# Kernel tuning notes

Measured on AMD Instinct MI355X. Metric: run time of the kernel, lower is better.

## Reference

```python
import jax, jax.numpy as jnp
import numpy as np

N = 100000   # nodes
E = 6400000  # edges (avg degree 64)
F = 512      # num_features
C = 16       # num_classes

def _glorot(key, shape):
    fan_in, fan_out = shape
    lim = (6.0 / (fan_in + fan_out)) ** 0.5
    return jax.random.uniform(key, shape, jnp.float32, -lim, lim)

def setup_inputs() -> dict:
    key = jax.random.key(0)
    ks = jax.random.split(key, 8)
    x = jax.random.normal(ks[0], (N, F), jnp.float32)
    edge_index = jax.random.randint(ks[1], (2, E), 0, N, dtype=jnp.int64)
    return {
        "x": x,
        "edge_index": edge_index,
        "W1": _glorot(ks[2], (F, 16)), "b1": jnp.zeros((16,), jnp.float32),
        "W2": _glorot(ks[3], (16, 32)), "b2": jnp.zeros((32,), jnp.float32),
        "W3": _glorot(ks[4], (32, C)),  "b3": jnp.zeros((C,), jnp.float32),
        "Wc": _glorot(ks[5], (C, C)),   "bc": jnp.zeros((C,), jnp.float32),
    }

def _gcn_conv(x, row, col, norm, W, b):
    # PyG GCNConv: transform, then normalized sum-aggregation, then bias
    h = x @ W                                   # [N, out]
    msg = h[row] * norm[:, None]                # gather + scale, [E+N, out]
    agg = jax.ops.segment_sum(msg, col, num_segments=N)
    return agg + b

def reference(x, edge_index, W1, b1, W2, b2, W3, b3, Wc, bc):
    n = x.shape[0]
    loops = jnp.arange(n, dtype=edge_index.dtype)
    row = jnp.concatenate([edge_index[0], loops])  # source
    col = jnp.concatenate([edge_index[1], loops])  # target
    # symmetric normalization D^{-1/2} A_hat D^{-1/2}
    deg = jax.ops.segment_sum(jnp.ones_like(col, dtype=x.dtype), col, num_segments=n)
    dis = jnp.where(deg > 0, jax.lax.rsqrt(deg), 0.0)
    norm = dis[row] * dis[col]                     # [E+N]
    h = jax.nn.relu(_gcn_conv(x, row, col, norm, W1, b1))
    h = jax.nn.relu(_gcn_conv(h, row, col, norm, W2, b2))
    h = jax.nn.relu(_gcn_conv(h, row, col, norm, W3, b3))
    out = h @ Wc + bc
    return (out, h)
```

## Files before the change

### kernel.cpp

```cpp
#include <hip/hip_runtime.h>
#include <hip/hip_bf16.h>
#include <hip/hip_fp16.h>
#include <stdint.h>


#define MS_CHUNK 15360

__device__ __forceinline__ int blockScanExclusive256(int v, int* wsum) {
  int lane = threadIdx.x & 63;
  int wid  = threadIdx.x >> 6;
  int inc = v;
#pragma unroll
  for (int d = 1; d < 64; d <<= 1) {
    int y = __shfl_up(inc, d, 64);
    if (lane >= d) inc += y;
  }
  if (lane == 63) wsum[wid] = inc;
  __syncthreads();
  if (threadIdx.x == 0) {
    int s = 0;
#pragma unroll
    for (int w = 0; w < 4; ++w) { int t = wsum[w]; wsum[w] = s; s += t; }
  }
  __syncthreads();
  return inc - v + wsum[wid];
}

__device__ __forceinline__ int blockScanExclusive512(int v, int* wsum) {
  int lane = threadIdx.x & 63;
  int wid  = threadIdx.x >> 6;
  int inc = v;
#pragma unroll
  for (int d = 1; d < 64; d <<= 1) {
    int y = __shfl_up(inc, d, 64);
    if (lane >= d) inc += y;
  }
  if (lane == 63) wsum[wid] = inc;
  __syncthreads();
  if (threadIdx.x == 0) {
    int s = 0;
#pragma unroll
    for (int w = 0; w < 8; ++w) { int t = wsum[w]; wsum[w] = s; s += t; }
  }
  __syncthreads();
  return inc - v + wsum[wid];
}

__global__ __launch_bounds__(256) void k_bscan(const int* __restrict__ counts,
                                               int* __restrict__ bbase,
                                               int nb, int etot) {
  __shared__ int wsum[4];
  __shared__ int carry_s;
  if (threadIdx.x == 0) carry_s = 0;
  __syncthreads();
  for (int base = 0; base < nb; base += 256) {
    int i = base + threadIdx.x;
    int v = (i < nb) ? counts[i] : 0;
    int ex = blockScanExclusive256(v, wsum);
    int c = carry_s;
    __syncthreads();
    if (i < nb) bbase[i] = ex + c;
    if (threadIdx.x == 255) carry_s = c + ex + v;
    __syncthreads();
  }
  if (threadIdx.x == 0) bbase[nb] = etot;
}

__global__ __launch_bounds__(256) void k_scatter1(
    const int* __restrict__ erow, const int* __restrict__ ecol,
    int* __restrict__ cursor, unsigned* __restrict__ sorted,
    int e, int chunk, int nb, int cap) {
  __shared__ unsigned staging[MS_CHUNK];
  __shared__ int lstart[256];
  __shared__ int lfill[256];
  __shared__ int gbase[256];
  __shared__ int wsum[4];
  int g = blockIdx.x;
  int s0 = g * chunk;
  int s1 = min(e, s0 + chunk);
  lfill[threadIdx.x] = 0;
  __syncthreads();
  {
    int i = s0 + threadIdx.x;
    for (; i + 768 < s1; i += 1024) {
      int c0 = ecol[i], c1 = ecol[i + 256], c2 = ecol[i + 512], c3 = ecol[i + 768];
      atomicAdd(&lfill[c0 >> 9], 1);
      atomicAdd(&lfill[c1 >> 9], 1);
      atomicAdd(&lfill[c2 >> 9], 1);
      atomicAdd(&lfill[c3 >> 9], 1);
    }
    for (; i < s1; i += 256) atomicAdd(&lfill[ecol[i] >> 9], 1);
  }
  __syncthreads();
  int cnt = lfill[threadIdx.x];
  int ex = blockScanExclusive256(cnt, wsum);
  lstart[threadIdx.x] = ex;
  int gb = 0;
  if (threadIdx.x < nb && cnt > 0) gb = atomicAdd(&cursor[threadIdx.x], cnt);
  gbase[threadIdx.x] = gb;
  __syncthreads();
  lfill[threadIdx.x] = 0;
  __syncthreads();
  {
    int i = s0 + threadIdx.x;
    for (; i + 768 < s1; i += 1024) {
      int c0 = ecol[i],       c1 = ecol[i + 256], c2 = ecol[i + 512], c3 = ecol[i + 768];
      int r0 = erow[i],       r1 = erow[i + 256], r2 = erow[i + 512], r3 = erow[i + 768];
      int b0 = c0 >> 9, b1 = c1 >> 9, b2 = c2 >> 9, b3 = c3 >> 9;
      int p0 = atomicAdd(&lfill[b0], 1);
      int p1 = atomicAdd(&lfill[b1], 1);
      int p2 = atomicAdd(&lfill[b2], 1);
      int p3 = atomicAdd(&lfill[b3], 1);
      staging[lstart[b0] + p0] = ((unsigned)r0 << 9) | (unsigned)(c0 & 511);
      staging[lstart[b1] + p1] = ((unsigned)r1 << 9) | (unsigned)(c1 & 511);
      staging[lstart[b2] + p2] = ((unsigned)r2 << 9) | (unsigned)(c2 & 511);
      staging[lstart[b3] + p3] = ((unsigned)r3 << 9) | (unsigned)(c3 & 511);
    }
    for (; i < s1; i += 256) {
      int c = ecol[i];
      int b = c >> 9;
      int p = atomicAdd(&lfill[b], 1);
      staging[lstart[b] + p] = ((unsigned)erow[i] << 9) | (unsigned)(c & 511);
    }
  }
  __syncthreads();
  int wid = threadIdx.x >> 6, L = threadIdx.x & 63;
  for (int b = wid; b < nb; b += 4) {
    int len = lfill[b];
    int ls = lstart[b];
    int gdst = b * cap + gbase[b];
    for (int j = L; j < len; j += 64)
      sorted[gdst + j] = staging[ls + j];
  }
}

__global__ __launch_bounds__(256) void k_transform1(
    const float* __restrict__ x, const float* __restrict__ W,
    __half* __restrict__ t1raw, int* __restrict__ cursor, int n) {
  if (blockIdx.x == 0) cursor[threadIdx.x] = 0;

  int L = threadIdx.x & 63;
  int wid = blockIdx.x * 4 + (threadIdx.x >> 6);
  int nw = gridDim.x * 4;

  float w[8][16];
  const float4* W4 = reinterpret_cast<const float4*>(W);
#pragma unroll
  for (int i = 0; i < 4; ++i) {
#pragma unroll
    for (int c4 = 0; c4 < 4; ++c4) {
      float4 va = W4[(4 * L + i) * 4 + c4];
      w[i][c4 * 4 + 0] = va.x; w[i][c4 * 4 + 1] = va.y;
      w[i][c4 * 4 + 2] = va.z; w[i][c4 * 4 + 3] = va.w;
      float4 vb = W4[(256 + 4 * L + i) * 4 + c4];
      w[4 + i][c4 * 4 + 0] = vb.x; w[4 + i][c4 * 4 + 1] = vb.y;
      w[4 + i][c4 * 4 + 2] = vb.z; w[4 + i][c4 * 4 + 3] = vb.w;
    }
  }
  int col = ((L & 1) << 3) | ((L & 2) << 1) | ((L & 4) >> 1) | ((L & 8) >> 3);

  for (int r = wid; r < n; r += nw) {
    const float4* xr = reinterpret_cast<const float4*>(x + (size_t)r * 512);
    float4 v0 = xr[L];
    float4 v1 = xr[64 + L];
    float acc[16];
#pragma unroll
    for (int c = 0; c < 16; ++c) {
      float a = v0.x * w[0][c];
      a = fmaf(v0.y, w[1][c], a);
      a = fmaf(v0.z, w[2][c], a);
      a = fmaf(v0.w, w[3][c], a);
      a = fmaf(v1.x, w[4][c], a);
      a = fmaf(v1.y, w[5][c], a);
      a = fmaf(v1.z, w[6][c], a);
      a = fmaf(v1.w, w[7][c], a);
      acc[c] = a;
    }
#pragma unroll
    for (int j = 0; j < 8; ++j) {
      float send = (L & 1) ? acc[j] : acc[j + 8];
      float recv = __shfl_xor(send, 1, 64);
      acc[j] = ((L & 1) ? acc[j + 8] : acc[j]) + recv;
    }
#pragma unroll
    for (int j = 0; j < 4; ++j) {
      float send = (L & 2) ? acc[j] : acc[j + 4];
      float recv = __shfl_xor(send, 2, 64);
      acc[j] = ((L & 2) ? acc[j + 4] : acc[j]) + recv;
    }
#pragma unroll
    for (int j = 0; j < 2; ++j) {
      float send = (L & 4) ? acc[j] : acc[j + 2];
      float recv = __shfl_xor(send, 4, 64);
      acc[j] = ((L & 4) ? acc[j + 2] : acc[j]) + recv;
    }
    {
      float send = (L & 8) ? acc[0] : acc[1];
      float recv = __shfl_xor(send, 8, 64);
      acc[0] = ((L & 8) ? acc[1] : acc[0]) + recv;
    }
    float s = acc[0];
    s += __shfl_xor(s, 16, 64);
    s += __shfl_xor(s, 32, 64);
    if (L < 16) t1raw[r * 16 + col] = __float2half(s);
  }
}

__global__ __launch_bounds__(512) void k_pass2(const unsigned* __restrict__ sorted,
                                               const int* __restrict__ counts,
                                               const int* __restrict__ bbase,
                                               float* __restrict__ dis,
                                               int* __restrict__ rowptr,
                                               __half* __restrict__ t1,
                                               int* __restrict__ csr,
                                               int n, int etot, int cap) {
  __shared__ int hist[512];
  __shared__ int cur[512];
  __shared__ int wsum[8];
  int b = blockIdx.x;
  hist[threadIdx.x] = 0;
  __syncthreads();
  int s0 = b * cap;
  int s1 = s0 + counts[b];
  for (int i = s0 + threadIdx.x; i < s1; i += 512)
    atomicAdd(&hist[sorted[i] & 511], 1);
  __syncthreads();
  int j = threadIdx.x;
  int node = (b << 9) + j;
  int deg = hist[j];
  int ex = blockScanExclusive512(deg, wsum);
  float dv = rsqrtf((float)(deg + 1));
  int gpos = bbase[b] + ex;
  cur[j] = gpos;
  if (node < n) {
    dis[node] = dv;
    rowptr[node] = gpos;
    __half2* t2 = reinterpret_cast<__half2*>(t1 + ((size_t)node << 4));
#pragma unroll
    for (int q = 0; q < 8; ++q) {
      float2 fv = __half22float2(t2[q]);
      fv.x *= dv; fv.y *= dv;
      t2[q] = __float22half2_rn(fv);
    }
  }
  if (b == 0 && threadIdx.x == 0) rowptr[n] = etot;
  __syncthreads();
  for (int i = s0 + threadIdx.x; i < s1; i += 512) {
    unsigned v = sorted[i];
    int pos = atomicAdd(&cur[v & 511], 1);
    csr[pos] = (int)(v >> 9);
  }
}

__device__ __forceinline__ float gather16(const __half* __restrict__ hs,
                                          const int* __restrict__ rowptr,
                                          const int* __restrict__ csr,
                                          int node, int f) {
  int base = (int)(threadIdx.x & 48);
  float acc0 = __half2float(hs[(node << 4) + f]);
  int e0 = rowptr[node], e1 = rowptr[node + 1];
  int e = e0;
  float acc1 = 0.f, acc2 = 0.f, acc3 = 0.f;
  for (; e + 16 <= e1; e += 16) {
    int rr = csr[e + f];
    int r0  = __shfl(rr, base + 0, 64),  r1  = __shfl(rr, base + 1, 64);
    int r2  = __shfl(rr, base + 2, 64),  r3  = __shfl(rr, base + 3, 64);
    int r4  = __shfl(rr, base + 4, 64),  r5  = __shfl(rr, base + 5, 64);
    int r6  = __shfl(rr, base + 6, 64),  r7  = __shfl(rr, base + 7, 64);
    int r8  = __shfl(rr, base + 8, 64),  r9  = __shfl(rr, base + 9, 64);
    int r10 = __shfl(rr, base + 10, 64), r11 = __shfl(rr, base + 11, 64);
    int r12 = __shfl(rr, base + 12, 64), r13 = __shfl(rr, base + 13, 64);
    int r14 = __shfl(rr, base + 14, 64), r15 = __shfl(rr, base + 15, 64);
    __half v0  = hs[(r0  << 4) + f], v1  = hs[(r1  << 4) + f];
    __half v2  = hs[(r2  << 4) + f], v3  = hs[(r3  << 4) + f];
    __half v4  = hs[(r4  << 4) + f], v5  = hs[(r5  << 4) + f];
    __half v6  = hs[(r6  << 4) + f], v7  = hs[(r7  << 4) + f];
    __half v8  = hs[(r8  << 4) + f], v9  = hs[(r9  << 4) + f];
    __half v10 = hs[(r10 << 4) + f], v11 = hs[(r11 << 4) + f];
    __half v12 = hs[(r12 << 4) + f], v13 = hs[(r13 << 4) + f];
    __half v14 = hs[(r14 << 4) + f], v15 = hs[(r15 << 4) + f];
    acc0 += (__half2float(v0)  + __half2float(v1))  + (__half2float(v2)  + __half2float(v3));
    acc1 += (__half2float(v4)  + __half2float(v5))  + (__half2float(v6)  + __half2float(v7));
    acc2 += (__half2float(v8)  + __half2float(v9))  + (__half2float(v10) + __half2float(v11));
    acc3 += (__half2float(v12) + __half2float(v13)) + (__half2float(v14) + __half2float(v15));
  }
  for (; e + 4 <= e1; e += 4) {
    int r0 = csr[e + 0], r1 = csr[e + 1], r2 = csr[e + 2], r3 = csr[e + 3];
    float v0 = __half2float(hs[(r0 << 4) + f]), v1 = __half2float(hs[(r1 << 4) + f]);
    float v2 = __half2float(hs[(r2 << 4) + f]), v3 = __half2float(hs[(r3 << 4) + f]);
    acc0 += (v0 + v1) + (v2 + v3);
  }
  for (; e < e1; ++e) acc0 += __half2float(hs[(csr[e] << 4) + f]);
  return (acc0 + acc1) + (acc2 + acc3);
}

__global__ __launch_bounds__(256) void k_agg_rb(
    const __half* __restrict__ hs, const int* __restrict__ rowptr,
    const int* __restrict__ csr, const float* __restrict__ dis,
    const float* __restrict__ b, __half* __restrict__ out, int n) {
  int node = blockIdx.x * 16 + threadIdx.x / 16;
  int f = threadIdx.x % 16;
  if (node >= n) return;
  float acc = gather16(hs, rowptr, csr, node, f);
  float d = dis[node];
  float t = fmaxf(fmaf(d, acc, b[f]), 0.f);
  out[(node << 4) + f] = __float2half(t * d);
}

__global__ __launch_bounds__(256) void k_agg_mid(
    const __half* __restrict__ hs, const int* __restrict__ rowptr,
    const int* __restrict__ csr, const float* __restrict__ dis,
    const float* __restrict__ W2, const float* __restrict__ b2,
    const float* __restrict__ W3, __half* __restrict__ out, int n) {
  __shared__ float w2s[512];
  __shared__ float w3s[512];
  __shared__ float b2s[32];
  for (int i = threadIdx.x; i < 512; i += 256) { w2s[i] = W2[i]; w3s[i] = W3[i]; }
  if (threadIdx.x < 32) b2s[threadIdx.x] = b2[threadIdx.x];
  __syncthreads();
  int node = blockIdx.x * 16 + threadIdx.x / 16;
  int f = threadIdx.x % 16;
  if (node >= n) return;
  float acc = gather16(hs, rowptr, csr, node, f);
  float d = dis[node];
  float v = d * acc;
  int base = threadIdx.x & 48;
  float a0 = b2s[f], a1 = b2s[f + 16];
#pragma unroll
  for (int k = 0; k < 16; ++k) {
    float vk = __shfl(v, base + k, 64);
    a0 = fmaf(vk, w2s[k * 32 + f], a0);
    a1 = fmaf(vk, w2s[k * 32 + 16 + f], a1);
  }
  a0 = fmaxf(a0, 0.f);
  a1 = fmaxf(a1, 0.f);
  float t = 0.f;
#pragma unroll
  for (int c = 0; c < 16; ++c) {
    float h0 = __shfl(a0, base + c, 64);
    float h1 = __shfl(a1, base + c, 64);
    t = fmaf(h0, w3s[c * 16 + f], t);
    t = fmaf(h1, w3s[(c + 16) * 16 + f], t);
  }
  out[(node << 4) + f] = __float2half(t * d);
}

__global__ __launch_bounds__(256) void k_agg_out(
    const __half* __restrict__ hs, const int* __restrict__ rowptr,
    const int* __restrict__ csr, const float* __restrict__ dis,
    const float* __restrict__ b3, const float* __restrict__ Wc,
    const float* __restrict__ bc, float* __restrict__ outh,
    float* __restrict__ outc, int n) {
  __shared__ float wcs[256];
  __shared__ float b3s[16];
  __shared__ float bcs[16];
  if (threadIdx.x < 256) wcs[threadIdx.x] = Wc[threadIdx.x];
  if (threadIdx.x < 16) { b3s[threadIdx.x] = b3[threadIdx.x]; bcs[threadIdx.x] = bc[threadIdx.x]; }
  __syncthreads();
  int node = blockIdx.x * 16 + threadIdx.x / 16;
  int f = threadIdx.x % 16;
  if (node >= n) return;
  float acc = gather16(hs, rowptr, csr, node, f);
  float d = dis[node];
  float h = fmaxf(fmaf(d, acc, b3s[f]), 0.f);
  outh[(node << 4) + f] = h;
  int base = threadIdx.x & 48;
  float o = bcs[f];
#pragma unroll
  for (int k = 0; k < 16; ++k) {
    float hk = __shfl(h, base + k, 64);
    o = fmaf(hk, wcs[k * 16 + f], o);
  }
  outc[(node << 4) + f] = o;
}

extern "C" void kernel_launch(void* const* d_in, const int* in_sizes, int n_in,
                              void* d_out, int out_size, void* d_ws, size_t ws_size,
                              hipStream_t stream) {
  (void)n_in; (void)out_size;
  const float* x  = (const float*)d_in[0];
  const int*   ei = (const int*)d_in[1];
  const float* W1 = (const float*)d_in[2];
  const float* b1 = (const float*)d_in[3];
  const float* W2 = (const float*)d_in[4];
  const float* b2 = (const float*)d_in[5];
  const float* W3 = (const float*)d_in[6];
  const float* b3 = (const float*)d_in[7];
  const float* Wc = (const float*)d_in[8];
  const float* bc = (const float*)d_in[9];

  const int F = 512;
  int N = in_sizes[0] / F;
  int E = in_sizes[1] / 2;
  const int* erow = ei;
  const int* ecol = ei + E;
  int NB = (N + 511) >> 9;
  const int chunk = MS_CHUNK;
  int GS = (E + chunk - 1) / chunk;
  int CAP = ((E / NB) + 2048 + 511) & ~511;

  auto align = [](size_t v) { return (v + 255) & ~(size_t)255; };
  char* p = (char*)d_ws;
  int*   cursor = (int*)p;   p += align(256 * 4);
  int*   bbase  = (int*)p;   p += align(257 * 4);
  float* dis    = (float*)p; p += align((size_t)N * 4);
  int*   rowptr = (int*)p;   p += align(((size_t)N + 1) * 4);
  int*   csr    = (int*)p;   p += align((size_t)E * 4);
  unsigned* sorted = (unsigned*)p; p += align((size_t)NB * CAP * 4);
  __half* bufA = (__half*)p; p += align((size_t)N * 16 * 2);
  __half* bufB = (__half*)p; p += align((size_t)N * 16 * 2);
  if ((size_t)(p - (char*)d_ws) > ws_size) return;

  float* outc = (float*)d_out;
  float* outh = (float*)d_out + (size_t)N * 16;

  k_transform1<<<2048, 256, 0, stream>>>(x, W1, bufA, cursor, N);
  k_scatter1<<<GS, 256, 0, stream>>>(erow, ecol, cursor, sorted, E, chunk, NB, CAP);
  k_bscan<<<1, 256, 0, stream>>>(cursor, bbase, NB, E);
  k_pass2<<<NB, 512, 0, stream>>>(sorted, cursor, bbase, dis, rowptr, bufA, csr, N, E, CAP);

  k_agg_rb<<<(N + 15) / 16, 256, 0, stream>>>(bufA, rowptr, csr, dis, b1, bufB, N);
  k_agg_mid<<<(N + 15) / 16, 256, 0, stream>>>(bufB, rowptr, csr, dis, W2, b2, W3, bufA, N);
  k_agg_out<<<(N + 15) / 16, 256, 0, stream>>>(bufA, rowptr, csr, dis, b3, Wc, bc, outh, outc, N);
}
```

Before: 317.7 us.

## Assign one wavefront per node in aggregation kernels instead of 16 lanes

The three aggregation kernels now map a full 64-lane wavefront to each destination node, with four edge slots of 16 features processed per step, and combine the partial sums with xor shuffles. The old scheme gave each node 16 lanes and a serial loop over neighbours. The change aims to raise the number of gathers in flight per node and reduce the serial loop length for degree-64 nodes. In exchange, each block covers 4× fewer nodes, there are extra reduction shuffles, and only 16 of 64 lanes write results.

```diff
diff --git a/kernel.cpp b/kernel.cpp
--- a/kernel.cpp
+++ b/kernel.cpp
@@ -252,59 +252,45 @@
   }
 }
 
-__device__ __forceinline__ float gather16(const __half* __restrict__ hs,
-                                          const int* __restrict__ rowptr,
-                                          const int* __restrict__ csr,
-                                          int node, int f) {
-  int base = (int)(threadIdx.x & 48);
-  float acc0 = __half2float(hs[(node << 4) + f]);
+__device__ __forceinline__ float gather_wave(const __half* __restrict__ hs,
+                                             const int* __restrict__ rowptr,
+                                             const int* __restrict__ csr,
+                                             int node, int L) {
+  int f = L & 15;
+  int es = L >> 4;
   int e0 = rowptr[node], e1 = rowptr[node + 1];
-  int e = e0;
-  float acc1 = 0.f, acc2 = 0.f, acc3 = 0.f;
-  for (; e + 16 <= e1; e += 16) {
-    int rr = csr[e + f];
-    int r0  = __shfl(rr, base + 0, 64),  r1  = __shfl(rr, base + 1, 64);
-    int r2  = __shfl(rr, base + 2, 64),  r3  = __shfl(rr, base + 3, 64);
-    int r4  = __shfl(rr, base + 4, 64),  r5  = __shfl(rr, base + 5, 64);
-    int r6  = __shfl(rr, base + 6, 64),  r7  = __shfl(rr, base + 7, 64);
-    int r8  = __shfl(rr, base + 8, 64),  r9  = __shfl(rr, base + 9, 64);
-    int r10 = __shfl(rr, base + 10, 64), r11 = __shfl(rr, base + 11, 64);
-    int r12 = __shfl(rr, base + 12, 64), r13 = __shfl(rr, base + 13, 64);
-    int r14 = __shfl(rr, base + 14, 64), r15 = __shfl(rr, base + 15, 64);
-    __half v0  = hs[(r0  << 4) + f], v1  = hs[(r1  << 4) + f];
-    __half v2  = hs[(r2  << 4) + f], v3  = hs[(r3  << 4) + f];
-    __half v4  = hs[(r4  << 4) + f], v5  = hs[(r5  << 4) + f];
-    __half v6  = hs[(r6  << 4) + f], v7  = hs[(r7  << 4) + f];
-    __half v8  = hs[(r8  << 4) + f], v9  = hs[(r9  << 4) + f];
-    __half v10 = hs[(r10 << 4) + f], v11 = hs[(r11 << 4) + f];
-    __half v12 = hs[(r12 << 4) + f], v13 = hs[(r13 << 4) + f];
-    __half v14 = hs[(r14 << 4) + f], v15 = hs[(r15 << 4) + f];
-    acc0 += (__half2float(v0)  + __half2float(v1))  + (__half2float(v2)  + __half2float(v3));
-    acc1 += (__half2float(v4)  + __half2float(v5))  + (__half2float(v6)  + __half2float(v7));
-    acc2 += (__half2float(v8)  + __half2float(v9))  + (__half2float(v10) + __half2float(v11));
-    acc3 += (__half2float(v12) + __half2float(v13)) + (__half2float(v14) + __half2float(v15));
-  }
-  for (; e + 4 <= e1; e += 4) {
-    int r0 = csr[e + 0], r1 = csr[e + 1], r2 = csr[e + 2], r3 = csr[e + 3];
-    float v0 = __half2float(hs[(r0 << 4) + f]), v1 = __half2float(hs[(r1 << 4) + f]);
-    float v2 = __half2float(hs[(r2 << 4) + f]), v3 = __half2float(hs[(r3 << 4) + f]);
-    acc0 += (v0 + v1) + (v2 + v3);
-  }
-  for (; e < e1; ++e) acc0 += __half2float(hs[(csr[e] << 4) + f]);
-  return (acc0 + acc1) + (acc2 + acc3);
+  float a0 = 0.f, a1 = 0.f, a2 = 0.f, a3 = 0.f;
+  for (int e = e0; e < e1; e += 16) {
+    int m = e + f;
+    int rr = (m < e1) ? csr[m] : 0;
+    int s0i = __shfl(rr, es, 64);
+    int s1i = __shfl(rr, 4 + es, 64);
+    int s2i = __shfl(rr, 8 + es, 64);
+    int s3i = __shfl(rr, 12 + es, 64);
+    if (e + es < e1)      a0 += __half2float(hs[(s0i << 4) + f]);
+    if (e + 4 + es < e1)  a1 += __half2float(hs[(s1i << 4) + f]);
+    if (e + 8 + es < e1)  a2 += __half2float(hs[(s2i << 4) + f]);
+    if (e + 12 + es < e1) a3 += __half2float(hs[(s3i << 4) + f]);
+  }
+  float acc = (a0 + a1) + (a2 + a3);
+  acc += __shfl_xor(acc, 16, 64);
+  acc += __shfl_xor(acc, 32, 64);
+  acc += __half2float(hs[(node << 4) + f]);
+  return acc;
 }
 
 __global__ __launch_bounds__(256) void k_agg_rb(
     const __half* __restrict__ hs, const int* __restrict__ rowptr,
     const int* __restrict__ csr, const float* __restrict__ dis,
     const float* __restrict__ b, __half* __restrict__ out, int n) {
-  int node = blockIdx.x * 16 + threadIdx.x / 16;
-  int f = threadIdx.x % 16;
+  int L = threadIdx.x & 63;
+  int node = blockIdx.x * 4 + (threadIdx.x >> 6);
   if (node >= n) return;
-  float acc = gather16(hs, rowptr, csr, node, f);
+  float acc = gather_wave(hs, rowptr, csr, node, L);
   float d = dis[node];
+  int f = L & 15;
   float t = fmaxf(fmaf(d, acc, b[f]), 0.f);
-  out[(node << 4) + f] = __float2half(t * d);
+  if (L < 16) out[(node << 4) + f] = __float2half(t * d);
 }
 
 __global__ __launch_bounds__(256) void k_agg_mid(
@@ -318,31 +304,28 @@
   for (int i = threadIdx.x; i < 512; i += 256) { w2s[i] = W2[i]; w3s[i] = W3[i]; }
   if (threadIdx.x < 32) b2s[threadIdx.x] = b2[threadIdx.x];
   __syncthreads();
-  int node = blockIdx.x * 16 + threadIdx.x / 16;
-  int f = threadIdx.x % 16;
+  int L = threadIdx.x & 63;
+  int node = blockIdx.x * 4 + (threadIdx.x >> 6);
   if (node >= n) return;
-  float acc = gather16(hs, rowptr, csr, node, f);
+  float acc = gather_wave(hs, rowptr, csr, node, L);
   float d = dis[node];
   float v = d * acc;
-  int base = threadIdx.x & 48;
-  float a0 = b2s[f], a1 = b2s[f + 16];
+  int f2 = L & 31;
+  float a = b2s[f2];
 #pragma unroll
   for (int k = 0; k < 16; ++k) {
-    float vk = __shfl(v, base + k, 64);
-    a0 = fmaf(vk, w2s[k * 32 + f], a0);
-    a1 = fmaf(vk, w2s[k * 32 + 16 + f], a1);
-  }
-  a0 = fmaxf(a0, 0.f);
-  a1 = fmaxf(a1, 0.f);
+    float vk = __shfl(v, k, 64);
+    a = fmaf(vk, w2s[k * 32 + f2], a);
+  }
+  a = fmaxf(a, 0.f);
+  int f = L & 15;
   float t = 0.f;
 #pragma unroll
-  for (int c = 0; c < 16; ++c) {
-    float h0 = __shfl(a0, base + c, 64);
-    float h1 = __shfl(a1, base + c, 64);
-    t = fmaf(h0, w3s[c * 16 + f], t);
-    t = fmaf(h1, w3s[(c + 16) * 16 + f], t);
-  }
-  out[(node << 4) + f] = __float2half(t * d);
+  for (int c = 0; c < 32; ++c) {
+    float hc = __shfl(a, c, 64);
+    t = fmaf(hc, w3s[c * 16 + f], t);
+  }
+  if (L < 16) out[(node << 4) + f] = __float2half(t * d);
 }
 
 __global__ __launch_bounds__(256) void k_agg_out(
@@ -357,21 +340,21 @@
   if (threadIdx.x < 256) wcs[threadIdx.x] = Wc[threadIdx.x];
   if (threadIdx.x < 16) { b3s[threadIdx.x] = b3[threadIdx.x]; bcs[threadIdx.x] = bc[threadIdx.x]; }
   __syncthreads();
-  int node = blockIdx.x * 16 + threadIdx.x / 16;
-  int f = threadIdx.x % 16;
+  int L = threadIdx.x & 63;
+  int node = blockIdx.x * 4 + (threadIdx.x >> 6);
   if (node >= n) return;
-  float acc = gather16(hs, rowptr, csr, node, f);
+  float acc = gather_wave(hs, rowptr, csr, node, L);
   float d = dis[node];
+  int f = L & 15;
   float h = fmaxf(fmaf(d, acc, b3s[f]), 0.f);
-  outh[(node << 4) + f] = h;
-  int base = threadIdx.x & 48;
+  if (L < 16) outh[(node << 4) + f] = h;
   float o = bcs[f];
 #pragma unroll
   for (int k = 0; k < 16; ++k) {
-    float hk = __shfl(h, base + k, 64);
+    float hk = __shfl(h, k, 64);
     o = fmaf(hk, wcs[k * 16 + f], o);
   }
-  outc[(node << 4) + f] = o;
+  if (L < 16) outc[(node << 4) + f] = o;
 }
 
 extern "C" void kernel_launch(void* const* d_in, const int* in_sizes, int n_in,
@@ -419,7 +402,8 @@
   k_bscan<<<1, 256, 0, stream>>>(cursor, bbase, NB, E);
   k_pass2<<<NB, 512, 0, stream>>>(sorted, cursor, bbase, dis, rowptr, bufA, csr, N, E, CAP);
 
-  k_agg_rb<<<(N + 15) / 16, 256, 0, stream>>>(bufA, rowptr, csr, dis, b1, bufB, N);
-  k_agg_mid<<<(N + 15) / 16, 256, 0, stream>>>(bufB, rowptr, csr, dis, W2, b2, W3, bufA, N);
-  k_agg_out<<<(N + 15) / 16, 256, 0, stream>>>(bufA, rowptr, csr, dis, b3, Wc, bc, outh, outc, N);
-}
+  int nblk = (N + 3) / 4;
+  k_agg_rb<<<nblk, 256, 0, stream>>>(bufA, rowptr, csr, dis, b1, bufB, N);
+  k_agg_mid<<<nblk, 256, 0, stream>>>(bufB, rowptr, csr, dis, W2, b2, W3, bufA, N);
+  k_agg_out<<<nblk, 256, 0, stream>>>(bufA, rowptr, csr, dis, b3, Wc, bc, outh, outc, N);
+}
```

Measured after the change: 476.9 us. +50.1%, slower.
